# Kernel tuning notes

Hardware: AMD Instinct MI355X
Metric: run time of the kernel (lower is better)

The kernel has to match this reference:

```python
import jax, jax.numpy as jnp
import numpy as np

HIDDEN = 1024


def setup_inputs() -> dict:
    key = jax.random.key(0)
    ks = jax.random.split(key, 9)
    B, S, Kq, H = 16, 4096, 64, HIDDEN
    scale = 1.0 / np.sqrt(H)
    return {
        "queries": jax.random.normal(ks[0], (B, Kq, H), jnp.float32),
        "keys": jax.random.normal(ks[1], (B, S, H), jnp.float32),
        "values": jax.random.normal(ks[2], (B, S, H), jnp.float32),
        "Wq": jax.random.normal(ks[3], (H, H), jnp.float32) * scale,
        "bq": jax.random.normal(ks[4], (H,), jnp.float32) * 0.02,
        "Wk": jax.random.normal(ks[5], (H, H), jnp.float32) * scale,
        "bk": jax.random.normal(ks[6], (H,), jnp.float32) * 0.02,
        "Wv": jax.random.normal(ks[7], (H, H), jnp.float32) * scale,
        "bv": jax.random.normal(ks[8], (H,), jnp.float32) * 0.02,
    }


def reference(queries, keys, values, Wq, bq, Wk, bk, Wv, bv):
    H = Wq.shape[0]
    scaling = jax.lax.rsqrt(jnp.asarray(H, queries.dtype))
    # torch Linear: x @ W^T + b
    q = queries @ Wq.T + bq            # (B, Kq, H)
    k = keys @ Wk.T + bk               # (B, S, H)
    v = values @ Wv.T + bv             # (B, S, H)
    # scores: k @ q^T -> (B, S, Kq), softmax over seq_len axis (dim=1)
    scores = jnp.einsum('bsh,bqh->bsq', k, q) * scaling
    attention_weights = jax.nn.softmax(scores, axis=1)
    # context: attn^T @ v -> (B, Kq, H)
    context = jnp.einsum('bsq,bsh->bqh', attention_weights, v)
    return context, attention_weights
```

## Files before the change

kernel.cpp:

```cpp
#include <hip/hip_runtime.h>
#include <hip/hip_bf16.h>

#define H 1024
#define SEQ 4096
#define BQ 64
#define NB 16

typedef float f32x4 __attribute__((ext_vector_type(4)));
typedef __bf16 bf16x8 __attribute__((ext_vector_type(8)));

__device__ __forceinline__ void split_bf16(const float* x, bf16x8& hi, bf16x8& lo)
{
    #pragma unroll
    for (int i = 0; i < 8; ++i) {
        float v = x[i];
        __bf16 h = (__bf16)v;
        hi[i] = h;
        lo[i] = (__bf16)(v - (float)h);
    }
}

__global__ __launch_bounds__(256)
void mfma_gemm_bt(const float* __restrict__ A, const float* __restrict__ Bm,
                  const float* __restrict__ bias, float* __restrict__ C, float scale)
{
    const int m0 = blockIdx.x * 64;
    const int n0 = blockIdx.y * 64;
    const int w   = threadIdx.x >> 6;
    const int l   = threadIdx.x & 63;
    const int row = l & 15;
    const int kg  = l >> 4;

    const float* ap = A + (size_t)(m0 + w * 16 + row) * H + kg * 8;
    const float* bp = Bm + (size_t)(n0 + row) * H + kg * 8;

    f32x4 acc[4] = {};
    for (int k0 = 0; k0 < H; k0 += 32) {
        float a8[8];
        *reinterpret_cast<float4*>(&a8[0]) = *reinterpret_cast<const float4*>(ap + k0);
        *reinterpret_cast<float4*>(&a8[4]) = *reinterpret_cast<const float4*>(ap + k0 + 4);
        bf16x8 ahi, alo;
        split_bf16(a8, ahi, alo);
        #pragma unroll
        for (int j = 0; j < 4; ++j) {
            float b8[8];
            const float* bjp = bp + (size_t)j * 16 * H + k0;
            *reinterpret_cast<float4*>(&b8[0]) = *reinterpret_cast<const float4*>(bjp);
            *reinterpret_cast<float4*>(&b8[4]) = *reinterpret_cast<const float4*>(bjp + 4);
            bf16x8 bhi, blo;
            split_bf16(b8, bhi, blo);
            acc[j] = __builtin_amdgcn_mfma_f32_16x16x32_bf16(ahi, bhi, acc[j], 0, 0, 0);
            acc[j] = __builtin_amdgcn_mfma_f32_16x16x32_bf16(ahi, blo, acc[j], 0, 0, 0);
            acc[j] = __builtin_amdgcn_mfma_f32_16x16x32_bf16(alo, bhi, acc[j], 0, 0, 0);
        }
    }
    #pragma unroll
    for (int j = 0; j < 4; ++j) {
        int n = n0 + j * 16 + row;
        float bb = bias ? bias[n] : 0.f;
        #pragma unroll
        for (int r = 0; r < 4; ++r) {
            int m = m0 + w * 16 + kg * 4 + r;
            C[(size_t)m * H + n] = acc[j][r] * scale + bb;
        }
    }
}

__global__ __launch_bounds__(256)
void ngemm_mfma(const float* __restrict__ q, const float* __restrict__ Wk,
                __bf16* __restrict__ Nhi, __bf16* __restrict__ Nlo, float scale)
{
    const int m0 = blockIdx.x * 64;
    const int n0 = blockIdx.y * 64;
    const int w   = threadIdx.x >> 6;
    const int l   = threadIdx.x & 63;
    const int row = l & 15;
    const int kg  = l >> 4;

    const float* ap = q + (size_t)(m0 + w * 16 + row) * H + kg * 8;
    const float* bp = Wk + (size_t)(kg * 8) * H + n0 + row;

    f32x4 acc[4] = {};
    for (int k0 = 0; k0 < H; k0 += 32) {
        float a8[8];
        *reinterpret_cast<float4*>(&a8[0]) = *reinterpret_cast<const float4*>(ap + k0);
        *reinterpret_cast<float4*>(&a8[4]) = *reinterpret_cast<const float4*>(ap + k0 + 4);
        bf16x8 ahi, alo;
        split_bf16(a8, ahi, alo);
        #pragma unroll
        for (int j = 0; j < 4; ++j) {
            float b8[8];
            #pragma unroll
            for (int e = 0; e < 8; ++e)
                b8[e] = bp[(size_t)(k0 + e) * H + j * 16];
            bf16x8 bhi, blo;
            split_bf16(b8, bhi, blo);
            acc[j] = __builtin_amdgcn_mfma_f32_16x16x32_bf16(ahi, bhi, acc[j], 0, 0, 0);
            acc[j] = __builtin_amdgcn_mfma_f32_16x16x32_bf16(ahi, blo, acc[j], 0, 0, 0);
            acc[j] = __builtin_amdgcn_mfma_f32_16x16x32_bf16(alo, bhi, acc[j], 0, 0, 0);
        }
    }
    #pragma unroll
    for (int j = 0; j < 4; ++j) {
        int n = n0 + j * 16 + row;
        #pragma unroll
        for (int r = 0; r < 4; ++r) {
            int m = m0 + w * 16 + kg * 4 + r;
            float v = acc[j][r] * scale;
            __bf16 hi = (__bf16)v;
            Nhi[(size_t)m * H + n] = hi;
            Nlo[(size_t)m * H + n] = (__bf16)(v - (float)hi);
        }
    }
}

__global__ __launch_bounds__(256)
void cvec_kernel(const float* __restrict__ q, const float* __restrict__ bk,
                 float* __restrict__ cvec, float scale)
{
    int r = blockIdx.x * 4 + (threadIdx.x >> 6);
    int l = threadIdx.x & 63;
    float s = 0.f;
    #pragma unroll
    for (int i = 0; i < 16; ++i)
        s += q[(size_t)r * H + l + 64 * i] * bk[l + 64 * i];
    #pragma unroll
    for (int off = 32; off; off >>= 1)
        s += __shfl_down(s, off);
    if (l == 0) cvec[r] = s * scale;
}

__global__ __launch_bounds__(256)
void scores_mfma(const float* __restrict__ keys,
                 const __bf16* __restrict__ Nhi, const __bf16* __restrict__ Nlo,
                 const float* __restrict__ cvec, float* __restrict__ scores)
{
    const int id = blockIdx.x;
    const int x  = id & 7;
    const int m  = id >> 3;
    const int b  = 2 * x + (m >> 6);
    const int s0 = (m & 63) * 64;

    const int t   = threadIdx.x;
    const int w   = t >> 6;
    const int l   = t & 63;
    const int row = l & 15;
    const int kg  = l >> 4;

    __shared__ __bf16 nshH[64][16][8];
    __shared__ __bf16 nshL[64][16][8];

    const float* ka = keys + ((size_t)b * SEQ + s0 + w * 16 + row) * H + kg * 8;
    const __bf16* nhb = Nhi + (size_t)b * BQ * H;
    const __bf16* nlb = Nlo + (size_t)b * BQ * H;

    const int sqi = t >> 4;
    const int skb = t & 15;

    f32x4 acc[4] = {};
    for (int kc = 0; kc < H; kc += 128) {
        float4 kr[8];
        #pragma unroll
        for (int ii = 0; ii < 4; ++ii) {
            kr[2 * ii + 0] = *reinterpret_cast<const float4*>(ka + kc + ii * 32);
            kr[2 * ii + 1] = *reinterpret_cast<const float4*>(ka + kc + ii * 32 + 4);
        }
        bf16x8 nh[4], nl[4];
        #pragma unroll
        for (int rep = 0; rep < 4; ++rep) {
            size_t goff = (size_t)(rep * 16 + sqi) * H + kc + skb * 8;
            nh[rep] = *reinterpret_cast<const bf16x8*>(nhb + goff);
            nl[rep] = *reinterpret_cast<const bf16x8*>(nlb + goff);
        }
        __syncthreads();
        #pragma unroll
        for (int rep = 0; rep < 4; ++rep) {
            *reinterpret_cast<bf16x8*>(&nshH[rep * 16 + sqi][skb][0]) = nh[rep];
            *reinterpret_cast<bf16x8*>(&nshL[rep * 16 + sqi][skb][0]) = nl[rep];
        }
        __syncthreads();
        #pragma unroll
        for (int ii = 0; ii < 4; ++ii) {
            float a8[8];
            *reinterpret_cast<float4*>(&a8[0]) = kr[2 * ii + 0];
            *reinterpret_cast<float4*>(&a8[4]) = kr[2 * ii + 1];
            bf16x8 ahi, alo;
            split_bf16(a8, ahi, alo);
            const int kb = ii * 4 + kg;
            #pragma unroll
            for (int j = 0; j < 4; ++j) {
                bf16x8 bhi = *reinterpret_cast<const bf16x8*>(&nshH[j * 16 + row][kb][0]);
                bf16x8 blo = *reinterpret_cast<const bf16x8*>(&nshL[j * 16 + row][kb][0]);
                acc[j] = __builtin_amdgcn_mfma_f32_16x16x32_bf16(ahi, bhi, acc[j], 0, 0, 0);
                acc[j] = __builtin_amdgcn_mfma_f32_16x16x32_bf16(ahi, blo, acc[j], 0, 0, 0);
                acc[j] = __builtin_amdgcn_mfma_f32_16x16x32_bf16(alo, bhi, acc[j], 0, 0, 0);
            }
        }
    }
    #pragma unroll
    for (int j = 0; j < 4; ++j) {
        int qi = j * 16 + row;
        float c = cvec[b * BQ + qi];
        #pragma unroll
        for (int r = 0; r < 4; ++r) {
            int s = s0 + w * 16 + kg * 4 + r;
            scores[((size_t)b * SEQ + s) * BQ + qi] = acc[j][r] + c;
        }
    }
}

__global__ __launch_bounds__(256)
void sm_partial(const float* __restrict__ scores, float* __restrict__ pmax,
                float* __restrict__ psum)
{
    const int b  = blockIdx.y;
    const int ch = blockIdx.x;
    const int t  = threadIdx.x;
    const int qi = t & 63;
    const int g  = t >> 6;
    const float* sb = scores + ((size_t)b * SEQ + ch * 128) * BQ;
    float v[32];
    #pragma unroll
    for (int i = 0; i < 32; ++i)
        v[i] = sb[(size_t)(g + i * 4) * BQ + qi];
    float m = v[0];
    #pragma unroll
    for (int i = 1; i < 32; ++i) m = fmaxf(m, v[i]);
    __shared__ float red[4][64];
    red[g][qi] = m;
    __syncthreads();
    float M = fmaxf(fmaxf(red[0][qi], red[1][qi]), fmaxf(red[2][qi], red[3][qi]));
    float sum = 0.f;
    #pragma unroll
    for (int i = 0; i < 32; ++i) sum += __expf(v[i] - M);
    __syncthreads();
    red[g][qi] = sum;
    __syncthreads();
    if (g == 0) {
        float ssum = red[0][qi] + red[1][qi] + red[2][qi] + red[3][qi];
        pmax[((size_t)b * 32 + ch) * 64 + qi] = M;
        psum[((size_t)b * 32 + ch) * 64 + qi] = ssum;
    }
}

__global__ void sm_combine(const float* __restrict__ pmax,
                           const float* __restrict__ psum,
                           float* __restrict__ gstat)
{
    int b  = blockIdx.x;
    int qi = threadIdx.x;
    float m = -1e30f;
    for (int c = 0; c < 32; ++c)
        m = fmaxf(m, pmax[((size_t)b * 32 + c) * 64 + qi]);
    float s = 0.f;
    for (int c = 0; c < 32; ++c)
        s += psum[((size_t)b * 32 + c) * 64 + qi] *
             __expf(pmax[((size_t)b * 32 + c) * 64 + qi] - m);
    gstat[(size_t)b * 64 + qi] = m;
    gstat[(size_t)(NB + b) * 64 + qi] = 1.f / s;
}

__global__ __launch_bounds__(256)
void sm_norm(float* __restrict__ attn, const float* __restrict__ gstat,
             __hip_bfloat16* __restrict__ abfT)
{
    __shared__ float tile[64][133];
    const int b  = blockIdx.y;
    const int ch = blockIdx.x;
    const int t  = threadIdx.x;
    const int qi = t & 63;
    const int g  = t >> 6;
    const float M   = gstat[(size_t)b * 64 + qi];
    const float inv = gstat[(size_t)(NB + b) * 64 + qi];
    float* sb = attn + ((size_t)b * SEQ + ch * 128) * BQ;
    #pragma unroll 8
    for (int i = 0; i < 32; ++i) {
        int sl = g + i * 4;
        size_t idx = (size_t)sl * BQ + qi;
        float w = __expf(sb[idx] - M) * inv;
        sb[idx] = w;
        tile[qi][sl] = w;
    }
    __syncthreads();
    const int qo = t >> 2;
    const int c  = (t & 3) * 32;
    __hip_bfloat16* dst = abfT + ((size_t)(b * BQ + qo)) * SEQ + ch * 128 + c;
    #pragma unroll
    for (int v = 0; v < 4; ++v) {
        bf16x8 w8;
        #pragma unroll
        for (int e = 0; e < 8; ++e)
            w8[e] = (__bf16)tile[qo][c + v * 8 + e];
        *reinterpret_cast<bf16x8*>(dst + v * 8) = w8;
    }
}

__global__ __launch_bounds__(256)
void tmat_mfma(const __hip_bfloat16* __restrict__ abfT,
               const float* __restrict__ values,
               float* __restrict__ Tpart, int schunk)
{
    const int b   = blockIdx.z;
    const int sc  = blockIdx.y;
    const int h0  = blockIdx.x * 128;
    const int w   = threadIdx.x >> 6;
    const int l   = threadIdx.x & 63;
    const int row = l & 15;
    const int kg  = l >> 4;
    const int sbase = sc * schunk;

    const __hip_bfloat16* ap = abfT + ((size_t)b * BQ + row) * SEQ + sbase + kg * 8;
    const float* vp = values + ((size_t)b * SEQ + sbase + kg * 8) * H + h0 + w * 32 + row;

    f32x4 acc[4][2] = {};
    for (int k0 = 0; k0 < schunk; k0 += 32) {
        bf16x8 a[4];
        #pragma unroll
        for (int i = 0; i < 4; ++i)
            a[i] = *reinterpret_cast<const bf16x8*>(ap + (size_t)i * 16 * SEQ + k0);
        #pragma unroll
        for (int j = 0; j < 2; ++j) {
            float b8[8];
            const float* bp = vp + (size_t)k0 * H + j * 16;
            #pragma unroll
            for (int e = 0; e < 8; ++e) b8[e] = bp[(size_t)e * H];
            bf16x8 bhi, blo;
            split_bf16(b8, bhi, blo);
            #pragma unroll
            for (int i = 0; i < 4; ++i) {
                acc[i][j] = __builtin_amdgcn_mfma_f32_16x16x32_bf16(a[i], bhi, acc[i][j], 0, 0, 0);
                acc[i][j] = __builtin_amdgcn_mfma_f32_16x16x32_bf16(a[i], blo, acc[i][j], 0, 0, 0);
            }
        }
    }
    float* tp = Tpart + ((size_t)sc * NB + b) * BQ * H;
    #pragma unroll
    for (int i = 0; i < 4; ++i) {
        #pragma unroll
        for (int j = 0; j < 2; ++j) {
            int h = h0 + w * 32 + j * 16 + row;
            #pragma unroll
            for (int r = 0; r < 4; ++r) {
                int qi = i * 16 + kg * 4 + r;
                tp[(size_t)qi * H + h] = acc[i][j][r];
            }
        }
    }
}

template<int SC>
__global__ __launch_bounds__(256)
void tsum_kernel(float* __restrict__ Tpart)
{
    const size_t stride = (size_t)NB * BQ * H;
    size_t i = ((size_t)blockIdx.x * 256 + threadIdx.x) * 4;
    f32x4 s = *reinterpret_cast<const f32x4*>(Tpart + i);
    #pragma unroll
    for (int p = 1; p < SC; ++p)
        s += *reinterpret_cast<const f32x4*>(Tpart + p * stride + i);
    *reinterpret_cast<f32x4*>(Tpart + i) = s;
}

extern "C" void kernel_launch(void* const* d_in, const int* in_sizes, int n_in,
                              void* d_out, int out_size, void* d_ws, size_t ws_size,
                              hipStream_t stream)
{
    const float* queries = (const float*)d_in[0];
    const float* keys    = (const float*)d_in[1];
    const float* values  = (const float*)d_in[2];
    const float* Wq = (const float*)d_in[3];
    const float* bq = (const float*)d_in[4];
    const float* Wk = (const float*)d_in[5];
    const float* bk = (const float*)d_in[6];
    const float* Wv = (const float*)d_in[7];
    const float* bv = (const float*)d_in[8];

    float* out     = (float*)d_out;
    float* context = out;
    float* attn    = out + (size_t)NB * BQ * H;

    const int SC = (ws_size >= (41ull << 20)) ? 8 : 2;
    const int schunk = SEQ / SC;

    char* ws = (char*)d_ws;
    float* q     = (float*)ws;
    __bf16* Nhi  = (__bf16*)(ws + (4ull << 20));
    __bf16* Nlo  = (__bf16*)(ws + (6ull << 20));
    float* Tpart = (float*)ws;
    __hip_bfloat16* abfT = (__hip_bfloat16*)(ws + (size_t)SC * (4ull << 20));
    char* smalls = ws + (size_t)SC * (4ull << 20) + (8ull << 20);
    float* cvec  = (float*)smalls;
    float* gstat = (float*)(smalls + (64u << 10));
    float* pmax  = (float*)(smalls + (128u << 10));
    float* psum  = (float*)(smalls + (256u << 10));

    const float scale = 0.03125f;

    mfma_gemm_bt<<<dim3(16, 16), 256, 0, stream>>>(queries, Wq, bq, q, 1.0f);
    ngemm_mfma<<<dim3(16, 16), 256, 0, stream>>>(q, Wk, Nhi, Nlo, scale);
    cvec_kernel<<<256, 256, 0, stream>>>(q, bk, cvec, scale);
    scores_mfma<<<1024, 256, 0, stream>>>(keys, Nhi, Nlo, cvec, attn);
    sm_partial<<<dim3(32, NB), 256, 0, stream>>>(attn, pmax, psum);
    sm_combine<<<NB, 64, 0, stream>>>(pmax, psum, gstat);
    sm_norm<<<dim3(32, NB), 256, 0, stream>>>(attn, gstat, abfT);
    tmat_mfma<<<dim3(H / 128, SC, NB), 256, 0, stream>>>(abfT, values, Tpart, schunk);
    if (SC == 8) tsum_kernel<8><<<1024, 256, 0, stream>>>(Tpart);
    else         tsum_kernel<2><<<1024, 256, 0, stream>>>(Tpart);
    mfma_gemm_bt<<<dim3(16, 16), 256, 0, stream>>>(Tpart, Wv, bv, context, 1.0f);
}
```

Before: 299.7 us.

## Fuse softmax partials into scores kernel, pipeline its loads, transpose Wk, remap tmat grid

The per-chunk softmax max/sum reduction now happens in the scores kernel epilogue, so the separate sm_partial pass that re-read the scores is removed. The scores main loop is double-buffered with register prefetch and an XOR-swizzled shared layout to cut barriers and bank conflicts. Wk is transposed up front so the N-matrix GEMM can use vectorized row loads instead of strided scalar loads. The tmat launch also gets a flattened, remapped block index for better locality. In exchange it adds an extra transpose kernel and twice as many partial-stat chunks for the combine step.

New measurement: 313.5 us. 1.05x slower.

```diff
diff --git a/kernel.cpp b/kernel.cpp
--- a/kernel.cpp
+++ b/kernel.cpp
@@ -67,8 +67,38 @@
 }
 
 __global__ __launch_bounds__(256)
-void ngemm_mfma(const float* __restrict__ q, const float* __restrict__ Wk,
-                __bf16* __restrict__ Nhi, __bf16* __restrict__ Nlo, float scale)
+void transpose_k(const float* __restrict__ Wk, float* __restrict__ WkT)
+{
+    __shared__ float tile[64][65];
+    const int k0 = blockIdx.x * 64;
+    const int n0 = blockIdx.y * 64;
+    const int t  = threadIdx.x;
+    const int c4 = (t & 15) * 4;
+    const int r  = t >> 4;
+    #pragma unroll
+    for (int p = 0; p < 4; ++p) {
+        float4 v = *reinterpret_cast<const float4*>(&Wk[(size_t)(k0 + r + 16 * p) * H + n0 + c4]);
+        tile[r + 16 * p][c4 + 0] = v.x;
+        tile[r + 16 * p][c4 + 1] = v.y;
+        tile[r + 16 * p][c4 + 2] = v.z;
+        tile[r + 16 * p][c4 + 3] = v.w;
+    }
+    __syncthreads();
+    #pragma unroll
+    for (int p = 0; p < 4; ++p) {
+        int rr = r + 16 * p;
+        float4 o;
+        o.x = tile[c4 + 0][rr];
+        o.y = tile[c4 + 1][rr];
+        o.z = tile[c4 + 2][rr];
+        o.w = tile[c4 + 3][rr];
+        *reinterpret_cast<float4*>(&WkT[(size_t)(n0 + rr) * H + k0 + c4]) = o;
+    }
+}
+
+__global__ __launch_bounds__(256)
+void ngemm_bt(const float* __restrict__ A, const float* __restrict__ Bm,
+              __bf16* __restrict__ Nhi, __bf16* __restrict__ Nlo, float scale)
 {
     const int m0 = blockIdx.x * 64;
     const int n0 = blockIdx.y * 64;
@@ -77,8 +107,8 @@
     const int row = l & 15;
     const int kg  = l >> 4;
 
-    const float* ap = q + (size_t)(m0 + w * 16 + row) * H + kg * 8;
-    const float* bp = Wk + (size_t)(kg * 8) * H + n0 + row;
+    const float* ap = A + (size_t)(m0 + w * 16 + row) * H + kg * 8;
+    const float* bp = Bm + (size_t)(n0 + row) * H + kg * 8;
 
     f32x4 acc[4] = {};
     for (int k0 = 0; k0 < H; k0 += 32) {
@@ -90,9 +120,9 @@
         #pragma unroll
         for (int j = 0; j < 4; ++j) {
             float b8[8];
-            #pragma unroll
-            for (int e = 0; e < 8; ++e)
-                b8[e] = bp[(size_t)(k0 + e) * H + j * 16];
+            const float* bjp = bp + (size_t)j * 16 * H + k0;
+            *reinterpret_cast<float4*>(&b8[0]) = *reinterpret_cast<const float4*>(bjp);
+            *reinterpret_cast<float4*>(&b8[4]) = *reinterpret_cast<const float4*>(bjp + 4);
             bf16x8 bhi, blo;
             split_bf16(b8, bhi, blo);
             acc[j] = __builtin_amdgcn_mfma_f32_16x16x32_bf16(ahi, bhi, acc[j], 0, 0, 0);
@@ -133,13 +163,15 @@
 __global__ __launch_bounds__(256)
 void scores_mfma(const float* __restrict__ keys,
                  const __bf16* __restrict__ Nhi, const __bf16* __restrict__ Nlo,
-                 const float* __restrict__ cvec, float* __restrict__ scores)
+                 const float* __restrict__ cvec, float* __restrict__ scores,
+                 float* __restrict__ pmax, float* __restrict__ psum)
 {
     const int id = blockIdx.x;
     const int x  = id & 7;
     const int m  = id >> 3;
     const int b  = 2 * x + (m >> 6);
     const int s0 = (m & 63) * 64;
+    const int ch = m & 63;
 
     const int t   = threadIdx.x;
     const int w   = t >> 6;
@@ -147,99 +179,141 @@
     const int row = l & 15;
     const int kg  = l >> 4;
 
-    __shared__ __bf16 nshH[64][16][8];
-    __shared__ __bf16 nshL[64][16][8];
+    __shared__ __bf16 nshH[2][64][8][8];
+    __shared__ __bf16 nshL[2][64][8][8];
+    __shared__ float red[4][64];
 
     const float* ka = keys + ((size_t)b * SEQ + s0 + w * 16 + row) * H + kg * 8;
     const __bf16* nhb = Nhi + (size_t)b * BQ * H;
     const __bf16* nlb = Nlo + (size_t)b * BQ * H;
 
-    const int sqi = t >> 4;
-    const int skb = t & 15;
+    const int sqi  = t >> 2;
+    const int skb0 = (t & 3) * 2;
+
+    float4 kr[4];
+    bf16x8 nh[2], nl[2];
+    #pragma unroll
+    for (int ii = 0; ii < 2; ++ii) {
+        kr[2 * ii + 0] = *reinterpret_cast<const float4*>(ka + ii * 32);
+        kr[2 * ii + 1] = *reinterpret_cast<const float4*>(ka + ii * 32 + 4);
+    }
+    #pragma unroll
+    for (int u = 0; u < 2; ++u) {
+        size_t go = (size_t)sqi * H + (skb0 + u) * 8;
+        nh[u] = *reinterpret_cast<const bf16x8*>(nhb + go);
+        nl[u] = *reinterpret_cast<const bf16x8*>(nlb + go);
+    }
 
     f32x4 acc[4] = {};
-    for (int kc = 0; kc < H; kc += 128) {
-        float4 kr[8];
-        #pragma unroll
-        for (int ii = 0; ii < 4; ++ii) {
-            kr[2 * ii + 0] = *reinterpret_cast<const float4*>(ka + kc + ii * 32);
-            kr[2 * ii + 1] = *reinterpret_cast<const float4*>(ka + kc + ii * 32 + 4);
-        }
-        bf16x8 nh[4], nl[4];
-        #pragma unroll
-        for (int rep = 0; rep < 4; ++rep) {
-            size_t goff = (size_t)(rep * 16 + sqi) * H + kc + skb * 8;
-            nh[rep] = *reinterpret_cast<const bf16x8*>(nhb + goff);
-            nl[rep] = *reinterpret_cast<const bf16x8*>(nlb + goff);
+    #pragma unroll
+    for (int c = 0; c < 16; ++c) {
+        const int buf = c & 1;
+        #pragma unroll
+        for (int u = 0; u < 2; ++u) {
+            int kb = skb0 + u;
+            int slot = kb ^ (sqi & 7);
+            *reinterpret_cast<bf16x8*>(&nshH[buf][sqi][slot][0]) = nh[u];
+            *reinterpret_cast<bf16x8*>(&nshL[buf][sqi][slot][0]) = nl[u];
+        }
+        float4 krn[4];
+        bf16x8 nhn[2], nln[2];
+        if (c < 15) {
+            const int kc = (c + 1) * 64;
+            #pragma unroll
+            for (int ii = 0; ii < 2; ++ii) {
+                krn[2 * ii + 0] = *reinterpret_cast<const float4*>(ka + kc + ii * 32);
+                krn[2 * ii + 1] = *reinterpret_cast<const float4*>(ka + kc + ii * 32 + 4);
+            }
+            #pragma unroll
+            for (int u = 0; u < 2; ++u) {
+                size_t go = (size_t)sqi * H + kc + (skb0 + u) * 8;
+                nhn[u] = *reinterpret_cast<const bf16x8*>(nhb + go);
+                nln[u] = *reinterpret_cast<const bf16x8*>(nlb + go);
+            }
         }
         __syncthreads();
         #pragma unroll
-        for (int rep = 0; rep < 4; ++rep) {
-            *reinterpret_cast<bf16x8*>(&nshH[rep * 16 + sqi][skb][0]) = nh[rep];
-            *reinterpret_cast<bf16x8*>(&nshL[rep * 16 + sqi][skb][0]) = nl[rep];
-        }
-        __syncthreads();
-        #pragma unroll
-        for (int ii = 0; ii < 4; ++ii) {
+        for (int ii = 0; ii < 2; ++ii) {
             float a8[8];
             *reinterpret_cast<float4*>(&a8[0]) = kr[2 * ii + 0];
             *reinterpret_cast<float4*>(&a8[4]) = kr[2 * ii + 1];
             bf16x8 ahi, alo;
             split_bf16(a8, ahi, alo);
             const int kb = ii * 4 + kg;
+            const int slot = kb ^ (row & 7);
             #pragma unroll
             for (int j = 0; j < 4; ++j) {
-                bf16x8 bhi = *reinterpret_cast<const bf16x8*>(&nshH[j * 16 + row][kb][0]);
-                bf16x8 blo = *reinterpret_cast<const bf16x8*>(&nshL[j * 16 + row][kb][0]);
+                const int qi = j * 16 + row;
+                bf16x8 bhi = *reinterpret_cast<const bf16x8*>(&nshH[buf][qi][slot][0]);
+                bf16x8 blo = *reinterpret_cast<const bf16x8*>(&nshL[buf][qi][slot][0]);
                 acc[j] = __builtin_amdgcn_mfma_f32_16x16x32_bf16(ahi, bhi, acc[j], 0, 0, 0);
                 acc[j] = __builtin_amdgcn_mfma_f32_16x16x32_bf16(ahi, blo, acc[j], 0, 0, 0);
                 acc[j] = __builtin_amdgcn_mfma_f32_16x16x32_bf16(alo, bhi, acc[j], 0, 0, 0);
             }
         }
-    }
-    #pragma unroll
-    for (int j = 0; j < 4; ++j) {
-        int qi = j * 16 + row;
-        float c = cvec[b * BQ + qi];
+        if (c < 15) {
+            #pragma unroll
+            for (int z = 0; z < 4; ++z) kr[z] = krn[z];
+            #pragma unroll
+            for (int u = 0; u < 2; ++u) { nh[u] = nhn[u]; nl[u] = nln[u]; }
+        }
+    }
+
+    float cv[4];
+    #pragma unroll
+    for (int j = 0; j < 4; ++j) cv[j] = cvec[b * BQ + j * 16 + row];
+    #pragma unroll
+    for (int j = 0; j < 4; ++j) {
+        const int qi = j * 16 + row;
         #pragma unroll
         for (int r = 0; r < 4; ++r) {
+            acc[j][r] += cv[j];
             int s = s0 + w * 16 + kg * 4 + r;
-            scores[((size_t)b * SEQ + s) * BQ + qi] = acc[j][r] + c;
-        }
-    }
-}
-
-__global__ __launch_bounds__(256)
-void sm_partial(const float* __restrict__ scores, float* __restrict__ pmax,
-                float* __restrict__ psum)
-{
-    const int b  = blockIdx.y;
-    const int ch = blockIdx.x;
-    const int t  = threadIdx.x;
-    const int qi = t & 63;
-    const int g  = t >> 6;
-    const float* sb = scores + ((size_t)b * SEQ + ch * 128) * BQ;
-    float v[32];
-    #pragma unroll
-    for (int i = 0; i < 32; ++i)
-        v[i] = sb[(size_t)(g + i * 4) * BQ + qi];
-    float m = v[0];
-    #pragma unroll
-    for (int i = 1; i < 32; ++i) m = fmaxf(m, v[i]);
-    __shared__ float red[4][64];
-    red[g][qi] = m;
+            scores[((size_t)b * SEQ + s) * BQ + qi] = acc[j][r];
+        }
+    }
+    float mj[4];
+    #pragma unroll
+    for (int j = 0; j < 4; ++j) {
+        float m0 = fmaxf(fmaxf(acc[j][0], acc[j][1]), fmaxf(acc[j][2], acc[j][3]));
+        m0 = fmaxf(m0, __shfl_xor(m0, 16));
+        m0 = fmaxf(m0, __shfl_xor(m0, 32));
+        mj[j] = m0;
+    }
+    if (kg == 0) {
+        #pragma unroll
+        for (int j = 0; j < 4; ++j) red[w][j * 16 + row] = mj[j];
+    }
     __syncthreads();
-    float M = fmaxf(fmaxf(red[0][qi], red[1][qi]), fmaxf(red[2][qi], red[3][qi]));
-    float sum = 0.f;
-    #pragma unroll
-    for (int i = 0; i < 32; ++i) sum += __expf(v[i] - M);
+    #pragma unroll
+    for (int j = 0; j < 4; ++j) {
+        const int qi = j * 16 + row;
+        mj[j] = fmaxf(fmaxf(red[0][qi], red[1][qi]), fmaxf(red[2][qi], red[3][qi]));
+    }
+    float sj[4];
+    #pragma unroll
+    for (int j = 0; j < 4; ++j) {
+        float s = 0.f;
+        #pragma unroll
+        for (int r = 0; r < 4; ++r) s += __expf(acc[j][r] - mj[j]);
+        s += __shfl_xor(s, 16);
+        s += __shfl_xor(s, 32);
+        sj[j] = s;
+    }
     __syncthreads();
-    red[g][qi] = sum;
+    if (kg == 0) {
+        #pragma unroll
+        for (int j = 0; j < 4; ++j) red[w][j * 16 + row] = sj[j];
+    }
     __syncthreads();
-    if (g == 0) {
-        float ssum = red[0][qi] + red[1][qi] + red[2][qi] + red[3][qi];
-        pmax[((size_t)b * 32 + ch) * 64 + qi] = M;
-        psum[((size_t)b * 32 + ch) * 64 + qi] = ssum;
+    if (w == 0 && kg == 0) {
+        #pragma unroll
+        for (int j = 0; j < 4; ++j) {
+            const int qi = j * 16 + row;
+            pmax[((size_t)b * 64 + ch) * 64 + qi] = mj[j];
+            psum[((size_t)b * 64 + ch) * 64 + qi] =
+                red[0][qi] + red[1][qi] + red[2][qi] + red[3][qi];
+        }
     }
 }
 
@@ -250,12 +324,12 @@
     int b  = blockIdx.x;
     int qi = threadIdx.x;
     float m = -1e30f;
-    for (int c = 0; c < 32; ++c)
-        m = fmaxf(m, pmax[((size_t)b * 32 + c) * 64 + qi]);
+    for (int c = 0; c < 64; ++c)
+        m = fmaxf(m, pmax[((size_t)b * 64 + c) * 64 + qi]);
     float s = 0.f;
-    for (int c = 0; c < 32; ++c)
-        s += psum[((size_t)b * 32 + c) * 64 + qi] *
-             __expf(pmax[((size_t)b * 32 + c) * 64 + qi] - m);
+    for (int c = 0; c < 64; ++c)
+        s += psum[((size_t)b * 64 + c) * 64 + qi] *
+             __expf(pmax[((size_t)b * 64 + c) * 64 + qi] - m);
     gstat[(size_t)b * 64 + qi] = m;
     gstat[(size_t)(NB + b) * 64 + qi] = 1.f / s;
 }
@@ -295,14 +369,19 @@
     }
 }
 
+template<int SC>
 __global__ __launch_bounds__(256)
 void tmat_mfma(const __hip_bfloat16* __restrict__ abfT,
                const float* __restrict__ values,
-               float* __restrict__ Tpart, int schunk)
-{
-    const int b   = blockIdx.z;
-    const int sc  = blockIdx.y;
-    const int h0  = blockIdx.x * 128;
+               float* __restrict__ Tpart)
+{
+    const int i  = blockIdx.x;
+    const int h0 = ((i >> 3) & 7) * 128;
+    const int g  = (i & 7) + 8 * (i >> 6);
+    const int b  = g / SC;
+    const int sc = g % SC;
+    const int schunk = SEQ / SC;
+
     const int w   = threadIdx.x >> 6;
     const int l   = threadIdx.x & 63;
     const int row = l & 15;
@@ -316,8 +395,8 @@
     for (int k0 = 0; k0 < schunk; k0 += 32) {
         bf16x8 a[4];
         #pragma unroll
-        for (int i = 0; i < 4; ++i)
-            a[i] = *reinterpret_cast<const bf16x8*>(ap + (size_t)i * 16 * SEQ + k0);
+        for (int q = 0; q < 4; ++q)
+            a[q] = *reinterpret_cast<const bf16x8*>(ap + (size_t)q * 16 * SEQ + k0);
         #pragma unroll
         for (int j = 0; j < 2; ++j) {
             float b8[8];
@@ -327,22 +406,22 @@
             bf16x8 bhi, blo;
             split_bf16(b8, bhi, blo);
             #pragma unroll
-            for (int i = 0; i < 4; ++i) {
-                acc[i][j] = __builtin_amdgcn_mfma_f32_16x16x32_bf16(a[i], bhi, acc[i][j], 0, 0, 0);
-                acc[i][j] = __builtin_amdgcn_mfma_f32_16x16x32_bf16(a[i], blo, acc[i][j], 0, 0, 0);
+            for (int q = 0; q < 4; ++q) {
+                acc[q][j] = __builtin_amdgcn_mfma_f32_16x16x32_bf16(a[q], bhi, acc[q][j], 0, 0, 0);
+                acc[q][j] = __builtin_amdgcn_mfma_f32_16x16x32_bf16(a[q], blo, acc[q][j], 0, 0, 0);
             }
         }
     }
     float* tp = Tpart + ((size_t)sc * NB + b) * BQ * H;
     #pragma unroll
-    for (int i = 0; i < 4; ++i) {
+    for (int q = 0; q < 4; ++q) {
         #pragma unroll
         for (int j = 0; j < 2; ++j) {
             int h = h0 + w * 32 + j * 16 + row;
             #pragma unroll
             for (int r = 0; r < 4; ++r) {
-                int qi = i * 16 + kg * 4 + r;
-                tp[(size_t)qi * H + h] = acc[i][j][r];
+                int qi = q * 16 + kg * 4 + r;
+                tp[(size_t)qi * H + h] = acc[q][j][r];
             }
         }
     }
@@ -380,30 +459,31 @@
     float* attn    = out + (size_t)NB * BQ * H;
 
     const int SC = (ws_size >= (41ull << 20)) ? 8 : 2;
-    const int schunk = SEQ / SC;
 
     char* ws = (char*)d_ws;
     float* q     = (float*)ws;
-    __bf16* Nhi  = (__bf16*)(ws + (4ull << 20));
-    __bf16* Nlo  = (__bf16*)(ws + (6ull << 20));
+    float* WkT   = (float*)(ws + (4ull << 20));
+    __bf16* Nhi  = (__bf16*)(ws + (8ull << 20));
+    __bf16* Nlo  = (__bf16*)(ws + (10ull << 20));
     float* Tpart = (float*)ws;
     __hip_bfloat16* abfT = (__hip_bfloat16*)(ws + (size_t)SC * (4ull << 20));
     char* smalls = ws + (size_t)SC * (4ull << 20) + (8ull << 20);
     float* cvec  = (float*)smalls;
     float* gstat = (float*)(smalls + (64u << 10));
     float* pmax  = (float*)(smalls + (128u << 10));
-    float* psum  = (float*)(smalls + (256u << 10));
+    float* psum  = (float*)(smalls + (512u << 10));
 
     const float scale = 0.03125f;
 
+    transpose_k<<<dim3(16, 16), 256, 0, stream>>>(Wk, WkT);
     mfma_gemm_bt<<<dim3(16, 16), 256, 0, stream>>>(queries, Wq, bq, q, 1.0f);
-    ngemm_mfma<<<dim3(16, 16), 256, 0, stream>>>(q, Wk, Nhi, Nlo, scale);
+    ngemm_bt<<<dim3(16, 16), 256, 0, stream>>>(q, WkT, Nhi, Nlo, scale);
     cvec_kernel<<<256, 256, 0, stream>>>(q, bk, cvec, scale);
-    scores_mfma<<<1024, 256, 0, stream>>>(keys, Nhi, Nlo, cvec, attn);
-    sm_partial<<<dim3(32, NB), 256, 0, stream>>>(attn, pmax, psum);
+    scores_mfma<<<1024, 256, 0, stream>>>(keys, Nhi, Nlo, cvec, attn, pmax, psum);
     sm_combine<<<NB, 64, 0, stream>>>(pmax, psum, gstat);
     sm_norm<<<dim3(32, NB), 256, 0, stream>>>(attn, gstat, abfT);
-    tmat_mfma<<<dim3(H / 128, SC, NB), 256, 0, stream>>>(abfT, values, Tpart, schunk);
+    if (SC == 8) tmat_mfma<8><<<8 * NB * 8, 256, 0, stream>>>(abfT, values, Tpart);
+    else         tmat_mfma<2><<<8 * NB * 2, 256, 0, stream>>>(abfT, values, Tpart);
     if (SC == 8) tsum_kernel<8><<<1024, 256, 0, stream>>>(Tpart);
     else         tsum_kernel<2><<<1024, 256, 0, stream>>>(Tpart);
     mfma_gemm_bt<<<dim3(16, 16), 256, 0, stream>>>(Tpart, Wv, bv, context, 1.0f);
```

## Split-K scores kernel across waves, transpose Wk for coalesced N-gemm, remap tmat blocks

Applied to the files above, without the earlier changes.

The scores kernel now gives each block 32 sequence rows and splits the hidden dimension across the four waves. Each wave reads its N fragments straight from global memory instead of staging them in shared memory, and partial sums are reduced through LDS at the end. Wk is transposed up front so the N-gemm reads B with vectorized row loads instead of strided scalar loads. The tmat kernel gets a 1D block index remap intended to improve L2 locality of the values reads. The cost is an extra transpose launch and an LDS reduction, and the scores kernel now loads the N operands redundantly from global memory.

Result: slower. 535.2 us (+78.6%).

```diff
diff --git a/kernel.cpp b/kernel.cpp
--- a/kernel.cpp
+++ b/kernel.cpp
@@ -67,8 +67,38 @@
 }
 
 __global__ __launch_bounds__(256)
-void ngemm_mfma(const float* __restrict__ q, const float* __restrict__ Wk,
-                __bf16* __restrict__ Nhi, __bf16* __restrict__ Nlo, float scale)
+void transpose_k(const float* __restrict__ Wk, float* __restrict__ WkT)
+{
+    __shared__ float tile[64][65];
+    const int k0 = blockIdx.x * 64;
+    const int n0 = blockIdx.y * 64;
+    const int t  = threadIdx.x;
+    const int c4 = (t & 15) * 4;
+    const int r  = t >> 4;
+    #pragma unroll
+    for (int p = 0; p < 4; ++p) {
+        float4 v = *reinterpret_cast<const float4*>(&Wk[(size_t)(k0 + r + 16 * p) * H + n0 + c4]);
+        tile[r + 16 * p][c4 + 0] = v.x;
+        tile[r + 16 * p][c4 + 1] = v.y;
+        tile[r + 16 * p][c4 + 2] = v.z;
+        tile[r + 16 * p][c4 + 3] = v.w;
+    }
+    __syncthreads();
+    #pragma unroll
+    for (int p = 0; p < 4; ++p) {
+        int rr = r + 16 * p;
+        float4 o;
+        o.x = tile[c4 + 0][rr];
+        o.y = tile[c4 + 1][rr];
+        o.z = tile[c4 + 2][rr];
+        o.w = tile[c4 + 3][rr];
+        *reinterpret_cast<float4*>(&WkT[(size_t)(n0 + rr) * H + k0 + c4]) = o;
+    }
+}
+
+__global__ __launch_bounds__(256)
+void ngemm_bt(const float* __restrict__ A, const float* __restrict__ Bm,
+              __bf16* __restrict__ Nhi, __bf16* __restrict__ Nlo, float scale)
 {
     const int m0 = blockIdx.x * 64;
     const int n0 = blockIdx.y * 64;
@@ -77,8 +107,8 @@
     const int row = l & 15;
     const int kg  = l >> 4;
 
-    const float* ap = q + (size_t)(m0 + w * 16 + row) * H + kg * 8;
-    const float* bp = Wk + (size_t)(kg * 8) * H + n0 + row;
+    const float* ap = A + (size_t)(m0 + w * 16 + row) * H + kg * 8;
+    const float* bp = Bm + (size_t)(n0 + row) * H + kg * 8;
 
     f32x4 acc[4] = {};
     for (int k0 = 0; k0 < H; k0 += 32) {
@@ -90,9 +120,9 @@
         #pragma unroll
         for (int j = 0; j < 4; ++j) {
             float b8[8];
-            #pragma unroll
-            for (int e = 0; e < 8; ++e)
-                b8[e] = bp[(size_t)(k0 + e) * H + j * 16];
+            const float* bjp = bp + (size_t)j * 16 * H + k0;
+            *reinterpret_cast<float4*>(&b8[0]) = *reinterpret_cast<const float4*>(bjp);
+            *reinterpret_cast<float4*>(&b8[4]) = *reinterpret_cast<const float4*>(bjp + 4);
             bf16x8 bhi, blo;
             split_bf16(b8, bhi, blo);
             acc[j] = __builtin_amdgcn_mfma_f32_16x16x32_bf16(ahi, bhi, acc[j], 0, 0, 0);
@@ -138,8 +168,8 @@
     const int id = blockIdx.x;
     const int x  = id & 7;
     const int m  = id >> 3;
-    const int b  = 2 * x + (m >> 6);
-    const int s0 = (m & 63) * 64;
+    const int b  = 2 * x + (m >> 7);
+    const int s0 = (m & 127) * 32;
 
     const int t   = threadIdx.x;
     const int w   = t >> 6;
@@ -147,64 +177,69 @@
     const int row = l & 15;
     const int kg  = l >> 4;
 
-    __shared__ __bf16 nshH[64][16][8];
-    __shared__ __bf16 nshL[64][16][8];
-
-    const float* ka = keys + ((size_t)b * SEQ + s0 + w * 16 + row) * H + kg * 8;
-    const __bf16* nhb = Nhi + (size_t)b * BQ * H;
-    const __bf16* nlb = Nlo + (size_t)b * BQ * H;
-
-    const int sqi = t >> 4;
-    const int skb = t & 15;
-
-    f32x4 acc[4] = {};
-    for (int kc = 0; kc < H; kc += 128) {
-        float4 kr[8];
-        #pragma unroll
-        for (int ii = 0; ii < 4; ++ii) {
-            kr[2 * ii + 0] = *reinterpret_cast<const float4*>(ka + kc + ii * 32);
-            kr[2 * ii + 1] = *reinterpret_cast<const float4*>(ka + kc + ii * 32 + 4);
-        }
-        bf16x8 nh[4], nl[4];
-        #pragma unroll
-        for (int rep = 0; rep < 4; ++rep) {
-            size_t goff = (size_t)(rep * 16 + sqi) * H + kc + skb * 8;
-            nh[rep] = *reinterpret_cast<const bf16x8*>(nhb + goff);
-            nl[rep] = *reinterpret_cast<const bf16x8*>(nlb + goff);
-        }
-        __syncthreads();
-        #pragma unroll
-        for (int rep = 0; rep < 4; ++rep) {
-            *reinterpret_cast<bf16x8*>(&nshH[rep * 16 + sqi][skb][0]) = nh[rep];
-            *reinterpret_cast<bf16x8*>(&nshL[rep * 16 + sqi][skb][0]) = nl[rep];
-        }
-        __syncthreads();
-        #pragma unroll
-        for (int ii = 0; ii < 4; ++ii) {
+    const float*  ka0 = keys + ((size_t)b * SEQ + s0 + row) * H + kg * 8;
+    const __bf16* nhb = Nhi + ((size_t)b * BQ + row) * H + kg * 8;
+    const __bf16* nlb = Nlo + ((size_t)b * BQ + row) * H + kg * 8;
+    const int ksl = w * 256;
+
+    f32x4 acc[2][4] = {};
+    #pragma unroll
+    for (int kc = 0; kc < 8; ++kc) {
+        const int k0 = ksl + kc * 32;
+        bf16x8 bhi[4], blo[4];
+        #pragma unroll
+        for (int j = 0; j < 4; ++j) {
+            size_t off = (size_t)j * 16 * H + k0;
+            bhi[j] = *reinterpret_cast<const bf16x8*>(nhb + off);
+            blo[j] = *reinterpret_cast<const bf16x8*>(nlb + off);
+        }
+        #pragma unroll
+        for (int st = 0; st < 2; ++st) {
+            const float* ap = ka0 + (size_t)st * 16 * H + k0;
             float a8[8];
-            *reinterpret_cast<float4*>(&a8[0]) = kr[2 * ii + 0];
-            *reinterpret_cast<float4*>(&a8[4]) = kr[2 * ii + 1];
+            *reinterpret_cast<float4*>(&a8[0]) = *reinterpret_cast<const float4*>(ap);
+            *reinterpret_cast<float4*>(&a8[4]) = *reinterpret_cast<const float4*>(ap + 4);
             bf16x8 ahi, alo;
             split_bf16(a8, ahi, alo);
-            const int kb = ii * 4 + kg;
             #pragma unroll
             for (int j = 0; j < 4; ++j) {
-                bf16x8 bhi = *reinterpret_cast<const bf16x8*>(&nshH[j * 16 + row][kb][0]);
-                bf16x8 blo = *reinterpret_cast<const bf16x8*>(&nshL[j * 16 + row][kb][0]);
-                acc[j] = __builtin_amdgcn_mfma_f32_16x16x32_bf16(ahi, bhi, acc[j], 0, 0, 0);
-                acc[j] = __builtin_amdgcn_mfma_f32_16x16x32_bf16(ahi, blo, acc[j], 0, 0, 0);
-                acc[j] = __builtin_amdgcn_mfma_f32_16x16x32_bf16(alo, bhi, acc[j], 0, 0, 0);
+                acc[st][j] = __builtin_amdgcn_mfma_f32_16x16x32_bf16(ahi, bhi[j], acc[st][j], 0, 0, 0);
+                acc[st][j] = __builtin_amdgcn_mfma_f32_16x16x32_bf16(ahi, blo[j], acc[st][j], 0, 0, 0);
+                acc[st][j] = __builtin_amdgcn_mfma_f32_16x16x32_bf16(alo, bhi[j], acc[st][j], 0, 0, 0);
             }
         }
     }
-    #pragma unroll
-    for (int j = 0; j < 4; ++j) {
-        int qi = j * 16 + row;
-        float c = cvec[b * BQ + qi];
+
+    __shared__ f32x4 rbuf[3][8][64];
+    #pragma unroll
+    for (int st = 0; st < 2; ++st) {
+        #pragma unroll
+        for (int j = 0; j < 4; ++j) {
+            const int c  = st * 4 + j;
+            const int ow = st + 2 * (j >> 1);
+            if (ow != w) {
+                const int slot = (w < ow) ? w : w - 1;
+                rbuf[slot][c][l] = acc[st][j];
+            }
+        }
+    }
+    __syncthreads();
+    const int st = w & 1;
+    const int j0 = (w >> 1) * 2;
+    #pragma unroll
+    for (int jj = 0; jj < 2; ++jj) {
+        const int j = j0 + jj;
+        const int c = st * 4 + j;
+        f32x4 s = acc[st][j];
+        s += rbuf[0][c][l];
+        s += rbuf[1][c][l];
+        s += rbuf[2][c][l];
+        const int qi = j * 16 + row;
+        const float cv = cvec[b * BQ + qi];
         #pragma unroll
         for (int r = 0; r < 4; ++r) {
-            int s = s0 + w * 16 + kg * 4 + r;
-            scores[((size_t)b * SEQ + s) * BQ + qi] = acc[j][r] + c;
+            const int ss = s0 + st * 16 + kg * 4 + r;
+            scores[((size_t)b * SEQ + ss) * BQ + qi] = s[r] + cv;
         }
     }
 }
@@ -295,14 +330,19 @@
     }
 }
 
+template<int SC>
 __global__ __launch_bounds__(256)
 void tmat_mfma(const __hip_bfloat16* __restrict__ abfT,
                const float* __restrict__ values,
-               float* __restrict__ Tpart, int schunk)
-{
-    const int b   = blockIdx.z;
-    const int sc  = blockIdx.y;
-    const int h0  = blockIdx.x * 128;
+               float* __restrict__ Tpart)
+{
+    const int i  = blockIdx.x;
+    const int h0 = ((i >> 3) & 7) * 128;
+    const int g  = (i & 7) + 8 * (i >> 6);
+    const int b  = g / SC;
+    const int sc = g % SC;
+    const int schunk = SEQ / SC;
+
     const int w   = threadIdx.x >> 6;
     const int l   = threadIdx.x & 63;
     const int row = l & 15;
@@ -316,8 +356,8 @@
     for (int k0 = 0; k0 < schunk; k0 += 32) {
         bf16x8 a[4];
         #pragma unroll
-        for (int i = 0; i < 4; ++i)
-            a[i] = *reinterpret_cast<const bf16x8*>(ap + (size_t)i * 16 * SEQ + k0);
+        for (int q = 0; q < 4; ++q)
+            a[q] = *reinterpret_cast<const bf16x8*>(ap + (size_t)q * 16 * SEQ + k0);
         #pragma unroll
         for (int j = 0; j < 2; ++j) {
             float b8[8];
@@ -327,22 +367,22 @@
             bf16x8 bhi, blo;
             split_bf16(b8, bhi, blo);
             #pragma unroll
-            for (int i = 0; i < 4; ++i) {
-                acc[i][j] = __builtin_amdgcn_mfma_f32_16x16x32_bf16(a[i], bhi, acc[i][j], 0, 0, 0);
-                acc[i][j] = __builtin_amdgcn_mfma_f32_16x16x32_bf16(a[i], blo, acc[i][j], 0, 0, 0);
+            for (int q = 0; q < 4; ++q) {
+                acc[q][j] = __builtin_amdgcn_mfma_f32_16x16x32_bf16(a[q], bhi, acc[q][j], 0, 0, 0);
+                acc[q][j] = __builtin_amdgcn_mfma_f32_16x16x32_bf16(a[q], blo, acc[q][j], 0, 0, 0);
             }
         }
     }
     float* tp = Tpart + ((size_t)sc * NB + b) * BQ * H;
     #pragma unroll
-    for (int i = 0; i < 4; ++i) {
+    for (int q = 0; q < 4; ++q) {
         #pragma unroll
         for (int j = 0; j < 2; ++j) {
             int h = h0 + w * 32 + j * 16 + row;
             #pragma unroll
             for (int r = 0; r < 4; ++r) {
-                int qi = i * 16 + kg * 4 + r;
-                tp[(size_t)qi * H + h] = acc[i][j][r];
+                int qi = q * 16 + kg * 4 + r;
+                tp[(size_t)qi * H + h] = acc[q][j][r];
             }
         }
     }
@@ -380,30 +420,32 @@
     float* attn    = out + (size_t)NB * BQ * H;
 
     const int SC = (ws_size >= (41ull << 20)) ? 8 : 2;
-    const int schunk = SEQ / SC;
 
     char* ws = (char*)d_ws;
     float* q     = (float*)ws;
-    __bf16* Nhi  = (__bf16*)(ws + (4ull << 20));
-    __bf16* Nlo  = (__bf16*)(ws + (6ull << 20));
+    float* WkT   = (float*)(ws + (4ull << 20));
+    __bf16* Nhi  = (__bf16*)(ws + (8ull << 20));
+    __bf16* Nlo  = (__bf16*)(ws + (10ull << 20));
     float* Tpart = (float*)ws;
     __hip_bfloat16* abfT = (__hip_bfloat16*)(ws + (size_t)SC * (4ull << 20));
     char* smalls = ws + (size_t)SC * (4ull << 20) + (8ull << 20);
     float* cvec  = (float*)smalls;
     float* gstat = (float*)(smalls + (64u << 10));
     float* pmax  = (float*)(smalls + (128u << 10));
-    float* psum  = (float*)(smalls + (256u << 10));
+    float* psum  = (float*)(smalls + (512u << 10));
 
     const float scale = 0.03125f;
 
+    transpose_k<<<dim3(16, 16), 256, 0, stream>>>(Wk, WkT);
     mfma_gemm_bt<<<dim3(16, 16), 256, 0, stream>>>(queries, Wq, bq, q, 1.0f);
-    ngemm_mfma<<<dim3(16, 16), 256, 0, stream>>>(q, Wk, Nhi, Nlo, scale);
+    ngemm_bt<<<dim3(16, 16), 256, 0, stream>>>(q, WkT, Nhi, Nlo, scale);
     cvec_kernel<<<256, 256, 0, stream>>>(q, bk, cvec, scale);
-    scores_mfma<<<1024, 256, 0, stream>>>(keys, Nhi, Nlo, cvec, attn);
+    scores_mfma<<<2048, 256, 0, stream>>>(keys, Nhi, Nlo, cvec, attn);
     sm_partial<<<dim3(32, NB), 256, 0, stream>>>(attn, pmax, psum);
     sm_combine<<<NB, 64, 0, stream>>>(pmax, psum, gstat);
     sm_norm<<<dim3(32, NB), 256, 0, stream>>>(attn, gstat, abfT);
-    tmat_mfma<<<dim3(H / 128, SC, NB), 256, 0, stream>>>(abfT, values, Tpart, schunk);
+    if (SC == 8) tmat_mfma<8><<<8 * NB * 8, 256, 0, stream>>>(abfT, values, Tpart);
+    else         tmat_mfma<2><<<8 * NB * 2, 256, 0, stream>>>(abfT, values, Tpart);
     if (SC == 8) tsum_kernel<8><<<1024, 256, 0, stream>>>(Tpart);
     else         tsum_kernel<2><<<1024, 256, 0, stream>>>(Tpart);
     mfma_gemm_bt<<<dim3(16, 16), 256, 0, stream>>>(Tpart, Wv, bv, context, 1.0f);
```
